# Kernel tuning notes

Measured on AMD Instinct MI355X. Metric: run time of the kernel, lower is better.

## Reference

```python
import jax, jax.numpy as jnp
import numpy as np

N_NODES = 50000
E_DIR = 250000
IN_FEATS = 256
N_HIDDEN = 64
N_CLASSES = 40
HEADS = 4
NEG_SLOPE = 0.2


def _build_graph():
    # mirrors to_undirected(edge_index) then add_self_loops(...)
    rng = np.random.default_rng(0)
    s = rng.integers(0, N_NODES, E_DIR)
    d = rng.integers(0, N_NODES, E_DIR)
    edges = np.stack([np.concatenate([s, d]), np.concatenate([d, s])], axis=0)
    edges = np.unique(edges, axis=1)  # dedup, as to_undirected does
    loops = np.arange(N_NODES)
    src = np.concatenate([edges[0], loops]).astype(np.int32)
    dst = np.concatenate([edges[1], loops]).astype(np.int32)
    return jnp.asarray(src), jnp.asarray(dst)


def setup_inputs() -> dict:
    key = jax.random.key(0)
    ks = jax.random.split(key, 16)
    src, dst = _build_graph()
    x = jax.random.uniform(ks[0], (N_NODES, IN_FEATS), dtype=jnp.float32)
    scale = 0.05
    # layer 0: IN -> HEADS*N_HIDDEN
    W0 = jax.random.normal(ks[1], (IN_FEATS, HEADS * N_HIDDEN), dtype=jnp.float32) * scale
    al0 = jax.random.normal(ks[2], (HEADS, N_HIDDEN), dtype=jnp.float32) * scale
    ar0 = jax.random.normal(ks[3], (HEADS, N_HIDDEN), dtype=jnp.float32) * scale
    b0 = jnp.zeros((HEADS * N_HIDDEN,), dtype=jnp.float32)
    # layer 1: HEADS*N_HIDDEN -> HEADS*N_HIDDEN
    W1 = jax.random.normal(ks[4], (HEADS * N_HIDDEN, HEADS * N_HIDDEN), dtype=jnp.float32) * scale
    al1 = jax.random.normal(ks[5], (HEADS, N_HIDDEN), dtype=jnp.float32) * scale
    ar1 = jax.random.normal(ks[6], (HEADS, N_HIDDEN), dtype=jnp.float32) * scale
    b1 = jnp.zeros((HEADS * N_HIDDEN,), dtype=jnp.float32)
    # layer 2: HEADS*N_HIDDEN -> HEADS*N_CLASSES (mean over heads at the end)
    W2 = jax.random.normal(ks[7], (HEADS * N_HIDDEN, HEADS * N_CLASSES), dtype=jnp.float32) * scale
    al2 = jax.random.normal(ks[8], (HEADS, N_CLASSES), dtype=jnp.float32) * scale
    ar2 = jax.random.normal(ks[9], (HEADS, N_CLASSES), dtype=jnp.float32) * scale
    b2 = jnp.zeros((HEADS * N_CLASSES,), dtype=jnp.float32)
    return {"x": x, "src": src, "dst": dst,
            "W0": W0, "al0": al0, "ar0": ar0, "b0": b0,
            "W1": W1, "al1": al1, "ar1": ar1, "b1": b1,
            "W2": W2, "al2": al2, "ar2": ar2, "b2": b2}


def _gat_layer(h, W, al, ar, b, src, dst):
    # DGL GATConv (no dropout, no residual): fc -> per-head attention -> edge softmax -> scatter-sum
    n = h.shape[0]
    nh, f = al.shape
    feat = (h @ W).reshape(n, nh, f)                      # [N,H,F]
    el = jnp.einsum('nhf,hf->nh', feat, al)               # [N,H]
    er = jnp.einsum('nhf,hf->nh', feat, ar)               # [N,H]
    e = jax.nn.leaky_relu(el[src] + er[dst], NEG_SLOPE)   # [E,H]
    emax = jax.lax.stop_gradient(jax.ops.segment_max(e, dst, num_segments=n))
    ee = jnp.exp(e - emax[dst])
    denom = jax.ops.segment_sum(ee, dst, num_segments=n)  # [N,H], >0 (self-loops)
    alpha = ee / denom[dst]                               # edge softmax over incoming edges
    msg = feat[src] * alpha[:, :, None]                   # [E,H,F]
    out = jax.ops.segment_sum(msg, dst, num_segments=n)   # [N,H,F]
    return out + b.reshape(1, nh, f)


def reference(x, src, dst, W0, al0, ar0, b0, W1, al1, ar1, b1, W2, al2, ar2, b2):
    n = x.shape[0]
    # x.shape[1] != 8189 -> row-normalize with clamp(min=1)
    h = x / jnp.clip(jnp.sum(x, axis=1, keepdims=True), 1.0)
    h = jax.nn.elu(_gat_layer(h, W0, al0, ar0, b0, src, dst)).reshape(n, -1)
    h = jax.nn.elu(_gat_layer(h, W1, al1, ar1, b1, src, dst)).reshape(n, -1)
    logits = _gat_layer(h, W2, al2, ar2, b2, src, dst).mean(axis=1)  # mean over heads
    return jax.nn.log_softmax(logits, axis=1)
```

## Files before the change

### kernel.cpp

```cpp
#include <hip/hip_runtime.h>
#include <math.h>

#define HEADS 4
#define HID 64
#define NCLS 40
#define IN_FEATS 256
#define NEG_SLOPE 0.2f
#define CAP 64
#define FP8_S 256.0f

typedef __attribute__((ext_vector_type(8))) short short8;
typedef __attribute__((ext_vector_type(4))) float floatx4;
typedef __attribute__((ext_vector_type(2))) float floatx2;

__device__ __forceinline__ ushort f2bf(float x) {
    union { float f; unsigned u; } v; v.f = x;
    unsigned r = (v.u + 0x7fff + ((v.u >> 16) & 1)) >> 16;
    return (ushort)r;
}
__device__ __forceinline__ unsigned char f2fp8(float x) {
    int pk = __builtin_amdgcn_cvt_pk_fp8_f32(x, x, 0, false);
    return (unsigned char)(pk & 0xff);
}
__device__ __forceinline__ void gload_lds16(const void* g, void* l) {
    __builtin_amdgcn_global_load_lds(
        (const __attribute__((address_space(1))) void*)g,
        (__attribute__((address_space(3))) void*)l, 16, 0, 0);
}

__global__ __launch_bounds__(256) void k_prep(const int* __restrict__ src,
                                              int* __restrict__ rowptr, int Em, int rb,
                                              const float* __restrict__ W0,
                                              const float* __restrict__ W1,
                                              const float* __restrict__ W2,
                                              ushort* __restrict__ Wt0,
                                              ushort* __restrict__ Wt1,
                                              ushort* __restrict__ Wt2,
                                              const float* __restrict__ al0,
                                              const float* __restrict__ ar0,
                                              const float* __restrict__ al1,
                                              const float* __restrict__ ar1,
                                              const float* __restrict__ al2,
                                              const float* __restrict__ ar2,
                                              ushort* __restrict__ Wel,
                                              const float* __restrict__ x,
                                              ushort* __restrict__ A16, int n) {
    int b = blockIdx.x;
    if (b < rb) {
        int j = b * 256 + threadIdx.x;
        if (j <= Em) {
            if (j == 0) {
                int hi = src[0];
                for (int v = 0; v <= hi; ++v) rowptr[v] = 0;
            } else if (j == Em) {
                int lo = src[Em - 1];
                for (int v = lo + 1; v <= n; ++v) rowptr[v] = Em;
            } else {
                int a = src[j - 1], c = src[j];
                for (int v = a + 1; v <= c; ++v) rowptr[v] = j;
            }
        }
        return;
    }
    b -= rb;
    if (b < 256) {
        int idx = b * 256 + threadIdx.x;
        int k = idx >> 8, c = idx & 255;
        Wt0[c * 256 + k] = f2bf(W0[idx]);
        Wt1[c * 256 + k] = f2bf(W1[idx]);
        if (idx < 40960) {
            int k2 = idx / 160, c2 = idx - k2 * 160;
            Wt2[c2 * 256 + k2] = f2bf(W2[idx]);
        }
        return;
    }
    b -= 256;
    if (b < 24) {
        int idx = b * 256 + threadIdx.x;
        int l = idx >> 11;
        int r = (idx >> 8) & 7;
        int k = idx & 255;
        int h = r & 3;
        bool isr = (r >= 4);
        const float* W  = (l == 0) ? W0 : (l == 1) ? W1 : W2;
        const float* av = isr ? ((l == 0) ? ar0 : (l == 1) ? ar1 : ar2)
                              : ((l == 0) ? al0 : (l == 1) ? al1 : al2);
        int F  = (l == 2) ? 40 : 64;
        int NC = (l == 2) ? 160 : 256;
        const float* wrow = W + (size_t)k * NC + h * F;
        const float* arow = av + h * F;
        float sum = 0.f;
        for (int f = 0; f < F; ++f) sum += wrow[f] * arow[f];
        Wel[idx] = f2bf(sum);
        return;
    }
    b -= 24;
    int row = b * 4 + (threadIdx.x >> 6);
    if (row >= n) return;
    int lane = threadIdx.x & 63;
    float4 v = reinterpret_cast<const float4*>(x + (size_t)row * 256)[lane];
    float s = v.x + v.y + v.z + v.w;
    for (int off = 32; off; off >>= 1) s += __shfl_down(s, off);
    s = __shfl(s, 0);
    float inv = 1.0f / fmaxf(s, 1.0f);
    ushort4 o;
    o.x = f2bf(v.x * inv); o.y = f2bf(v.y * inv);
    o.z = f2bf(v.z * inv); o.w = f2bf(v.w * inv);
    reinterpret_cast<ushort4*>(A16 + (size_t)row * 256)[lane] = o;
}

#define LDK 64
#define LDW 264

__global__ __launch_bounds__(256) void k_gemm_mfma(const ushort* __restrict__ A16,
                                                   const ushort* __restrict__ Wt,
                                                   const ushort* __restrict__ Welg,
                                                   unsigned char* __restrict__ Out8,
                                                   float* __restrict__ elv,
                                                   float* __restrict__ erv,
                                                   int n, int NCOL) {
    __shared__ ushort As[128 * LDK];
    __shared__ ushort Bs[128 * LDK];
    __shared__ ushort Wls[16 * LDW];
    int t = threadIdx.x;
    int lane = t & 63;
    int w = t >> 6;
    int wrow = (w & 1) * 64;
    int wcol = (w >> 1) * 64;
    int row0 = blockIdx.x * 128;
    int col0 = blockIdx.y * 128;
    int lrow = lane & 15;
    int kq = lane >> 4;
    bool fuse_blk = (blockIdx.y == 0);

    if (fuse_blk) {
        int r = t >> 5;
        int kk = (t & 31) * 8;
        uint4 v = *reinterpret_cast<const uint4*>(&Welg[r * 256 + kk]);
        *reinterpret_cast<uint4*>(&Wls[r * LDW + kk]) = v;
        *reinterpret_cast<uint4*>(&Wls[(r + 8) * LDW + kk]) = make_uint4(0u, 0u, 0u, 0u);
    }

    floatx4 acc[4][4];
    floatx4 acc_e[4];
#pragma unroll
    for (int i = 0; i < 4; ++i) {
        acc_e[i] = (floatx4)(0.f);
#pragma unroll
        for (int j = 0; j < 4; ++j) acc[i][j] = (floatx4)(0.f);
    }

    for (int k0 = 0; k0 < 256; k0 += 64) {
#pragma unroll
        for (int p = 0; p < 4; ++p) {
            int idx = p * 256 + t;
            int r = idx >> 3;
            int kk = (idx & 7) * 8;
            int gr = row0 + r; gr = (gr < n) ? gr : (n - 1);
            gload_lds16(&A16[(size_t)gr * 256 + k0 + kk], &As[idx * 8]);
        }
#pragma unroll
        for (int p = 0; p < 4; ++p) {
            int idx = p * 256 + t;
            int c = idx >> 3;
            int kk = (idx & 7) * 8;
            int gc = col0 + c; gc = (gc < NCOL) ? gc : (NCOL - 1);
            gload_lds16(&Wt[(size_t)gc * 256 + k0 + kk], &Bs[idx * 8]);
        }
        __syncthreads();

#pragma unroll
        for (int kc = 0; kc < 2; ++kc) {
            int kb = kc * 32 + kq * 8;
            short8 af[4], bf[4];
#pragma unroll
            for (int i = 0; i < 4; ++i)
                af[i] = *reinterpret_cast<const short8*>(&As[(wrow + 16 * i + lrow) * LDK + kb]);
#pragma unroll
            for (int j = 0; j < 4; ++j)
                bf[j] = *reinterpret_cast<const short8*>(&Bs[(wcol + 16 * j + lrow) * LDK + kb]);
#pragma unroll
            for (int i = 0; i < 4; ++i)
#pragma unroll
                for (int j = 0; j < 4; ++j)
                    acc[i][j] = __builtin_amdgcn_mfma_f32_16x16x32_bf16(af[i], bf[j], acc[i][j], 0, 0, 0);
            if (fuse_blk && wcol == 0) {
                short8 bw = *reinterpret_cast<const short8*>(&Wls[lrow * LDW + kb]);
#pragma unroll
                for (int i = 0; i < 4; ++i)
                    acc_e[i] = __builtin_amdgcn_mfma_f32_16x16x32_bf16(af[i], bw, acc_e[i], 0, 0, 0);
            }
        }
        __syncthreads();
    }

#pragma unroll
    for (int j = 0; j < 4; ++j) {
        int c = col0 + wcol + 16 * j + lrow;
        if (c >= NCOL) continue;
#pragma unroll
        for (int i = 0; i < 4; ++i) {
            int rbase = row0 + wrow + 16 * i + kq * 4;
#pragma unroll
            for (int r = 0; r < 4; ++r) {
                int gr = rbase + r;
                if (gr < n) Out8[(size_t)gr * NCOL + c] = f2fp8(acc[i][j][r] * FP8_S);
            }
        }
    }
    if (fuse_blk && wcol == 0 && lrow < 8) {
        bool is_er = (lrow >= 4);
        int h = lrow & 3;
#pragma unroll
        for (int i = 0; i < 4; ++i) {
            int rbase = row0 + wrow + 16 * i + kq * 4;
#pragma unroll
            for (int r = 0; r < 4; ++r) {
                int gr = rbase + r;
                if (gr < n) {
                    float v = acc_e[i][r];
                    if (is_er) erv[gr * 4 + h] = v;
                    else       elv[gr * 4 + h] = v;
                }
            }
        }
    }
}

template <int Fh, bool FINAL>
__global__ __launch_bounds__(256) void k_agg9(const unsigned char* __restrict__ F8,
                                              const float* __restrict__ el,
                                              const float* __restrict__ er,
                                              const int* __restrict__ rowptr,
                                              const int* __restrict__ dstv,
                                              const float* __restrict__ bias,
                                              ushort* __restrict__ out16,
                                              float* __restrict__ outF,
                                              int n) {
    constexpr int RL = 4 * Fh;
    constexpr bool FULL = (RL == 256);
    __shared__ float wls[4][CAP * 4];
    __shared__ int   mls[4][CAP];
    __shared__ float fbuf[4][FINAL ? 160 : 1];
    int wid = threadIdx.x >> 6;
    int node = blockIdx.x * 4 + wid;
    if (node >= n) node = n - 1;
    int lane = threadIdx.x & 63;
    int lo = rowptr[node];
    int deg_main = rowptr[node + 1] - lo;
    if (deg_main > CAP - 1) deg_main = CAP - 1;
    int deg = deg_main + 1;
    int degp = (deg + 7) & ~7;

    float* wl = wls[wid];
    int*   ml = mls[wid];

    int h = lane & 3;
    float ern = er[node * 4 + h];
    float wr[4];
    float s = 0.f;
    int ecount = 0;
    for (int e = lane >> 2; e < deg; e += 16) {
        int mid = (e < deg_main) ? dstv[lo + e] : node;
        if (h == 0) ml[e] = mid;
        float x = el[mid * 4 + h] + ern;
        x = (x > 0.f) ? x : NEG_SLOPE * x;
        float w = __expf(x);
        wr[ecount++] = w;
        s += w;
    }
#pragma unroll
    for (int off = 4; off < 64; off <<= 1) s += __shfl_xor(s, off);
    float invd = (1.0f / FP8_S) / s;
    {
        int e = lane >> 2;
        for (int i = 0; i < ecount; ++i, e += 16) wl[e * 4 + h] = wr[i] * invd;
    }
    if (lane < degp - deg) {
        int e = deg + lane;
        ml[e] = node;
        wl[e * 4 + 0] = 0.f; wl[e * 4 + 1] = 0.f;
        wl[e * 4 + 2] = 0.f; wl[e * 4 + 3] = 0.f;
    }
    asm volatile("s_waitcnt lgkmcnt(0)" ::: "memory");

    int my = 4 * lane;
    bool act = FULL || (my < RL);
    int hB = FULL ? (lane >> 4) : (my / Fh);
    const unsigned char* F8my = F8 + my;
    float a0 = 0.f, a1 = 0.f, a2 = 0.f, a3 = 0.f;
    for (int j0 = 0; j0 < degp; j0 += 8) {
        int4 mA = *reinterpret_cast<const int4*>(&ml[j0]);
        int4 mB = *reinterpret_cast<const int4*>(&ml[j0 + 4]);
        float w0 = wl[(j0 + 0) * 4 + hB], w1 = wl[(j0 + 1) * 4 + hB];
        float w2 = wl[(j0 + 2) * 4 + hB], w3 = wl[(j0 + 3) * 4 + hB];
        float w4 = wl[(j0 + 4) * 4 + hB], w5 = wl[(j0 + 5) * 4 + hB];
        float w6 = wl[(j0 + 6) * 4 + hB], w7 = wl[(j0 + 7) * 4 + hB];
        unsigned u0 = 0u, u1 = 0u, u2 = 0u, u3 = 0u;
        unsigned u4 = 0u, u5 = 0u, u6 = 0u, u7 = 0u;
        if (act) {
            u0 = *reinterpret_cast<const unsigned*>(&F8my[(size_t)mA.x * RL]);
            u1 = *reinterpret_cast<const unsigned*>(&F8my[(size_t)mA.y * RL]);
            u2 = *reinterpret_cast<const unsigned*>(&F8my[(size_t)mA.z * RL]);
            u3 = *reinterpret_cast<const unsigned*>(&F8my[(size_t)mA.w * RL]);
            u4 = *reinterpret_cast<const unsigned*>(&F8my[(size_t)mB.x * RL]);
            u5 = *reinterpret_cast<const unsigned*>(&F8my[(size_t)mB.y * RL]);
            u6 = *reinterpret_cast<const unsigned*>(&F8my[(size_t)mB.z * RL]);
            u7 = *reinterpret_cast<const unsigned*>(&F8my[(size_t)mB.w * RL]);
        }
#define ACC_EDGE(U, W)                                                     \
        {                                                                  \
            floatx2 p01 = __builtin_amdgcn_cvt_pk_f32_fp8(U, false);       \
            floatx2 p23 = __builtin_amdgcn_cvt_pk_f32_fp8(U, true);        \
            a0 = fmaf(W, p01.x, a0); a1 = fmaf(W, p01.y, a1);              \
            a2 = fmaf(W, p23.x, a2); a3 = fmaf(W, p23.y, a3);              \
        }
        ACC_EDGE(u0, w0) ACC_EDGE(u1, w1) ACC_EDGE(u2, w2) ACC_EDGE(u3, w3)
        ACC_EDGE(u4, w4) ACC_EDGE(u5, w5) ACC_EDGE(u6, w6) ACC_EDGE(u7, w7)
#undef ACC_EDGE
    }

    if (!FINAL) {
        if (act) {
            float4 b4 = *reinterpret_cast<const float4*>(&bias[my]);
            float o0 = a0 + b4.x, o1 = a1 + b4.y, o2 = a2 + b4.z, o3 = a3 + b4.w;
            o0 = (o0 > 0.f) ? o0 : (__expf(o0) - 1.0f);
            o1 = (o1 > 0.f) ? o1 : (__expf(o1) - 1.0f);
            o2 = (o2 > 0.f) ? o2 : (__expf(o2) - 1.0f);
            o3 = (o3 > 0.f) ? o3 : (__expf(o3) - 1.0f);
            uint2 pk;
            pk.x = (unsigned)f2bf(o0) | ((unsigned)f2bf(o1) << 16);
            pk.y = (unsigned)f2bf(o2) | ((unsigned)f2bf(o3) << 16);
            *reinterpret_cast<uint2*>(&out16[(size_t)node * RL + my]) = pk;
        }
    } else {
        if (act) {
            float4 b4 = *reinterpret_cast<const float4*>(&bias[my]);
            fbuf[wid][my + 0] = a0 + b4.x;
            fbuf[wid][my + 1] = a1 + b4.y;
            fbuf[wid][my + 2] = a2 + b4.z;
            fbuf[wid][my + 3] = a3 + b4.w;
        }
        asm volatile("s_waitcnt lgkmcnt(0)" ::: "memory");
        float val = 0.f;
        if (lane < 40)
            val = 0.25f * (fbuf[wid][lane] + fbuf[wid][40 + lane] +
                           fbuf[wid][80 + lane] + fbuf[wid][120 + lane]);
        float mx = (lane < 40) ? val : -1e30f;
#pragma unroll
        for (int off = 32; off; off >>= 1) mx = fmaxf(mx, __shfl_xor(mx, off));
        float ex = (lane < 40) ? __expf(val - mx) : 0.f;
        float se = ex;
#pragma unroll
        for (int off = 32; off; off >>= 1) se += __shfl_xor(se, off);
        if (lane < 40) outF[(size_t)node * 40 + lane] = val - mx - logf(se);
    }
}

extern "C" void kernel_launch(void* const* d_in, const int* in_sizes, int n_in,
                              void* d_out, int out_size, void* d_ws, size_t ws_size,
                              hipStream_t stream) {
    const float* x  = (const float*)d_in[0];
    const int* src  = (const int*)d_in[1];
    const int* dst  = (const int*)d_in[2];
    const float* W0 = (const float*)d_in[3];
    const float* al0 = (const float*)d_in[4];
    const float* ar0 = (const float*)d_in[5];
    const float* b0 = (const float*)d_in[6];
    const float* W1 = (const float*)d_in[7];
    const float* al1 = (const float*)d_in[8];
    const float* ar1 = (const float*)d_in[9];
    const float* b1 = (const float*)d_in[10];
    const float* W2 = (const float*)d_in[11];
    const float* al2 = (const float*)d_in[12];
    const float* ar2 = (const float*)d_in[13];
    const float* b2 = (const float*)d_in[14];
    float* out = (float*)d_out;

    const int n = in_sizes[0] / IN_FEATS;
    const int E = in_sizes[1];
    const int Em = E - n;

    char* base = (char*)d_ws;
    size_t off = 0;
    auto alloc = [&](size_t bytes) {
        void* p = base + off;
        off = (off + bytes + 255) & ~(size_t)255;
        return p;
    };
    ushort* A16 = (ushort*)alloc((size_t)n * 256 * 2);
    unsigned char* F8 = (unsigned char*)alloc((size_t)n * 256);
    ushort* Wt0 = (ushort*)alloc((size_t)256 * 256 * 2);
    ushort* Wt1 = (ushort*)alloc((size_t)256 * 256 * 2);
    ushort* Wt2 = (ushort*)alloc((size_t)160 * 256 * 2);
    ushort* Wel = (ushort*)alloc((size_t)3 * 8 * 256 * 2);
    float* el  = (float*)alloc((size_t)n * HEADS * 4);
    float* er  = (float*)alloc((size_t)n * HEADS * 4);
    int* rowptr = (int*)alloc((size_t)(n + 1) * 4);
    (void)ws_size; (void)n_in; (void)out_size;

    const int rb = (Em + 1 + 255) / 256;
    const int nb4 = (n + 3) / 4;
    const int gemm_rows = (n + 127) / 128;

    k_prep<<<rb + 256 + 24 + nb4, 256, 0, stream>>>(src, rowptr, Em, rb,
                                                    W0, W1, W2, Wt0, Wt1, Wt2,
                                                    al0, ar0, al1, ar1, al2, ar2,
                                                    Wel, x, A16, n);

    k_gemm_mfma<<<dim3(gemm_rows, 2), 256, 0, stream>>>(A16, Wt0, Wel, F8, el, er, n, 256);
    k_agg9<HID, false><<<nb4, 256, 0, stream>>>(F8, el, er, rowptr, dst, b0, A16, out, n);

    k_gemm_mfma<<<dim3(gemm_rows, 2), 256, 0, stream>>>(A16, Wt1, Wel + 2048, F8, el, er, n, 256);
    k_agg9<HID, false><<<nb4, 256, 0, stream>>>(F8, el, er, rowptr, dst, b1, A16, out, n);

    k_gemm_mfma<<<dim3(gemm_rows, 2), 256, 0, stream>>>(A16, Wt2, Wel + 4096, F8, el, er, n, 160);
    k_agg9<NCLS, true><<<nb4, 256, 0, stream>>>(F8, el, er, rowptr, dst, b2, nullptr, out, n);
}
```

Measured before the change: 273.8 us.

## Split edges across half-waves with 8-byte FP8 gathers and software-pipelined loads

For the full-width (256-feature) aggregation layers, each lane now gathers 8 FP8 features per neighbor, and the two half-waves process alternating groups of 4 edges. Partial sums are combined with a cross-half shuffle. Loads for the next batch of edges are double-buffered so they overlap with the FMAs of the current batch. This aims to increase gather width and memory-level parallelism, at the cost of more registers, an extra shuffle reduction, and only half the lanes doing the epilogue.

```diff
diff --git a/kernel.cpp b/kernel.cpp
--- a/kernel.cpp
+++ b/kernel.cpp
@@ -284,56 +284,124 @@
     }
     asm volatile("s_waitcnt lgkmcnt(0)" ::: "memory");
 
-    int my = 4 * lane;
-    bool act = FULL || (my < RL);
-    int hB = FULL ? (lane >> 4) : (my / Fh);
-    const unsigned char* F8my = F8 + my;
-    float a0 = 0.f, a1 = 0.f, a2 = 0.f, a3 = 0.f;
-    for (int j0 = 0; j0 < degp; j0 += 8) {
-        int4 mA = *reinterpret_cast<const int4*>(&ml[j0]);
-        int4 mB = *reinterpret_cast<const int4*>(&ml[j0 + 4]);
-        float w0 = wl[(j0 + 0) * 4 + hB], w1 = wl[(j0 + 1) * 4 + hB];
-        float w2 = wl[(j0 + 2) * 4 + hB], w3 = wl[(j0 + 3) * 4 + hB];
-        float w4 = wl[(j0 + 4) * 4 + hB], w5 = wl[(j0 + 5) * 4 + hB];
-        float w6 = wl[(j0 + 6) * 4 + hB], w7 = wl[(j0 + 7) * 4 + hB];
-        unsigned u0 = 0u, u1 = 0u, u2 = 0u, u3 = 0u;
-        unsigned u4 = 0u, u5 = 0u, u6 = 0u, u7 = 0u;
-        if (act) {
-            u0 = *reinterpret_cast<const unsigned*>(&F8my[(size_t)mA.x * RL]);
-            u1 = *reinterpret_cast<const unsigned*>(&F8my[(size_t)mA.y * RL]);
-            u2 = *reinterpret_cast<const unsigned*>(&F8my[(size_t)mA.z * RL]);
-            u3 = *reinterpret_cast<const unsigned*>(&F8my[(size_t)mA.w * RL]);
-            u4 = *reinterpret_cast<const unsigned*>(&F8my[(size_t)mB.x * RL]);
-            u5 = *reinterpret_cast<const unsigned*>(&F8my[(size_t)mB.y * RL]);
-            u6 = *reinterpret_cast<const unsigned*>(&F8my[(size_t)mB.z * RL]);
-            u7 = *reinterpret_cast<const unsigned*>(&F8my[(size_t)mB.w * RL]);
-        }
-#define ACC_EDGE(U, W)                                                     \
-        {                                                                  \
-            floatx2 p01 = __builtin_amdgcn_cvt_pk_f32_fp8(U, false);       \
-            floatx2 p23 = __builtin_amdgcn_cvt_pk_f32_fp8(U, true);        \
-            a0 = fmaf(W, p01.x, a0); a1 = fmaf(W, p01.y, a1);              \
-            a2 = fmaf(W, p23.x, a2); a3 = fmaf(W, p23.y, a3);              \
-        }
-        ACC_EDGE(u0, w0) ACC_EDGE(u1, w1) ACC_EDGE(u2, w2) ACC_EDGE(u3, w3)
-        ACC_EDGE(u4, w4) ACC_EDGE(u5, w5) ACC_EDGE(u6, w6) ACC_EDGE(u7, w7)
-#undef ACC_EDGE
-    }
-
-    if (!FINAL) {
-        if (act) {
-            float4 b4 = *reinterpret_cast<const float4*>(&bias[my]);
-            float o0 = a0 + b4.x, o1 = a1 + b4.y, o2 = a2 + b4.z, o3 = a3 + b4.w;
+    if constexpr (FULL) {
+        int ep4 = (lane >> 5) << 2;
+        int c8 = (lane & 31) * 8;
+        int hB2 = c8 >> 6;
+        const unsigned char* F8c = F8 + c8;
+        float a0 = 0.f, a1 = 0.f, a2 = 0.f, a3 = 0.f;
+        float a4 = 0.f, a5 = 0.f, a6 = 0.f, a7 = 0.f;
+        int nb = degp >> 3;
+
+#define LOADB(J, MI, W0, W1, W2, W3, U0, U1, U2, U3)                        \
+        {                                                                   \
+            MI = *reinterpret_cast<const int4*>(&ml[(J) + ep4]);            \
+            W0 = wl[((J) + ep4 + 0) * 4 + hB2];                             \
+            W1 = wl[((J) + ep4 + 1) * 4 + hB2];                             \
+            W2 = wl[((J) + ep4 + 2) * 4 + hB2];                             \
+            W3 = wl[((J) + ep4 + 3) * 4 + hB2];                             \
+            U0 = *reinterpret_cast<const uint2*>(&F8c[(size_t)MI.x * 256]); \
+            U1 = *reinterpret_cast<const uint2*>(&F8c[(size_t)MI.y * 256]); \
+            U2 = *reinterpret_cast<const uint2*>(&F8c[(size_t)MI.z * 256]); \
+            U3 = *reinterpret_cast<const uint2*>(&F8c[(size_t)MI.w * 256]); \
+        }
+#define FMA8(W, U)                                                          \
+        {                                                                   \
+            floatx2 p01 = __builtin_amdgcn_cvt_pk_f32_fp8((U).x, false);    \
+            floatx2 p23 = __builtin_amdgcn_cvt_pk_f32_fp8((U).x, true);     \
+            floatx2 p45 = __builtin_amdgcn_cvt_pk_f32_fp8((U).y, false);    \
+            floatx2 p67 = __builtin_amdgcn_cvt_pk_f32_fp8((U).y, true);     \
+            a0 = fmaf(W, p01.x, a0); a1 = fmaf(W, p01.y, a1);               \
+            a2 = fmaf(W, p23.x, a2); a3 = fmaf(W, p23.y, a3);               \
+            a4 = fmaf(W, p45.x, a4); a5 = fmaf(W, p45.y, a5);               \
+            a6 = fmaf(W, p67.x, a6); a7 = fmaf(W, p67.y, a7);               \
+        }
+#define FMABATCH(W0, W1, W2, W3, U0, U1, U2, U3)                            \
+        { FMA8(W0, U0) FMA8(W1, U1) FMA8(W2, U2) FMA8(W3, U3) }
+
+        int4 miA, miB;
+        float wA0, wA1, wA2, wA3, wB0, wB1, wB2, wB3;
+        uint2 uA0, uA1, uA2, uA3, uB0, uB1, uB2, uB3;
+
+        LOADB(0, miA, wA0, wA1, wA2, wA3, uA0, uA1, uA2, uA3)
+        for (int b = 1; b < nb; ++b) {
+            int j0 = b * 8;
+            if (b & 1) {
+                LOADB(j0, miB, wB0, wB1, wB2, wB3, uB0, uB1, uB2, uB3)
+                FMABATCH(wA0, wA1, wA2, wA3, uA0, uA1, uA2, uA3)
+            } else {
+                LOADB(j0, miA, wA0, wA1, wA2, wA3, uA0, uA1, uA2, uA3)
+                FMABATCH(wB0, wB1, wB2, wB3, uB0, uB1, uB2, uB3)
+            }
+        }
+        if (nb & 1) { FMABATCH(wA0, wA1, wA2, wA3, uA0, uA1, uA2, uA3) }
+        else        { FMABATCH(wB0, wB1, wB2, wB3, uB0, uB1, uB2, uB3) }
+#undef FMABATCH
+#undef FMA8
+#undef LOADB
+
+        a0 += __shfl_xor(a0, 32); a1 += __shfl_xor(a1, 32);
+        a2 += __shfl_xor(a2, 32); a3 += __shfl_xor(a3, 32);
+        a4 += __shfl_xor(a4, 32); a5 += __shfl_xor(a5, 32);
+        a6 += __shfl_xor(a6, 32); a7 += __shfl_xor(a7, 32);
+
+        if (lane < 32) {
+            float4 b4a = *reinterpret_cast<const float4*>(&bias[c8]);
+            float4 b4b = *reinterpret_cast<const float4*>(&bias[c8 + 4]);
+            float o0 = a0 + b4a.x, o1 = a1 + b4a.y, o2 = a2 + b4a.z, o3 = a3 + b4a.w;
+            float o4 = a4 + b4b.x, o5 = a5 + b4b.y, o6 = a6 + b4b.z, o7 = a7 + b4b.w;
             o0 = (o0 > 0.f) ? o0 : (__expf(o0) - 1.0f);
             o1 = (o1 > 0.f) ? o1 : (__expf(o1) - 1.0f);
             o2 = (o2 > 0.f) ? o2 : (__expf(o2) - 1.0f);
             o3 = (o3 > 0.f) ? o3 : (__expf(o3) - 1.0f);
-            uint2 pk;
+            o4 = (o4 > 0.f) ? o4 : (__expf(o4) - 1.0f);
+            o5 = (o5 > 0.f) ? o5 : (__expf(o5) - 1.0f);
+            o6 = (o6 > 0.f) ? o6 : (__expf(o6) - 1.0f);
+            o7 = (o7 > 0.f) ? o7 : (__expf(o7) - 1.0f);
+            uint4 pk;
             pk.x = (unsigned)f2bf(o0) | ((unsigned)f2bf(o1) << 16);
             pk.y = (unsigned)f2bf(o2) | ((unsigned)f2bf(o3) << 16);
-            *reinterpret_cast<uint2*>(&out16[(size_t)node * RL + my]) = pk;
+            pk.z = (unsigned)f2bf(o4) | ((unsigned)f2bf(o5) << 16);
+            pk.w = (unsigned)f2bf(o6) | ((unsigned)f2bf(o7) << 16);
+            *reinterpret_cast<uint4*>(&out16[(size_t)node * RL + c8]) = pk;
         }
     } else {
+        int my = 4 * lane;
+        bool act = (my < RL);
+        int hB = my / Fh;
+        const unsigned char* F8my = F8 + my;
+        float a0 = 0.f, a1 = 0.f, a2 = 0.f, a3 = 0.f;
+        for (int j0 = 0; j0 < degp; j0 += 8) {
+            int4 mA = *reinterpret_cast<const int4*>(&ml[j0]);
+            int4 mB = *reinterpret_cast<const int4*>(&ml[j0 + 4]);
+            float w0 = wl[(j0 + 0) * 4 + hB], w1 = wl[(j0 + 1) * 4 + hB];
+            float w2 = wl[(j0 + 2) * 4 + hB], w3 = wl[(j0 + 3) * 4 + hB];
+            float w4 = wl[(j0 + 4) * 4 + hB], w5 = wl[(j0 + 5) * 4 + hB];
+            float w6 = wl[(j0 + 6) * 4 + hB], w7 = wl[(j0 + 7) * 4 + hB];
+            unsigned u0 = 0u, u1 = 0u, u2 = 0u, u3 = 0u;
+            unsigned u4 = 0u, u5 = 0u, u6 = 0u, u7 = 0u;
+            if (act) {
+                u0 = *reinterpret_cast<const unsigned*>(&F8my[(size_t)mA.x * RL]);
+                u1 = *reinterpret_cast<const unsigned*>(&F8my[(size_t)mA.y * RL]);
+                u2 = *reinterpret_cast<const unsigned*>(&F8my[(size_t)mA.z * RL]);
+                u3 = *reinterpret_cast<const unsigned*>(&F8my[(size_t)mA.w * RL]);
+                u4 = *reinterpret_cast<const unsigned*>(&F8my[(size_t)mB.x * RL]);
+                u5 = *reinterpret_cast<const unsigned*>(&F8my[(size_t)mB.y * RL]);
+                u6 = *reinterpret_cast<const unsigned*>(&F8my[(size_t)mB.z * RL]);
+                u7 = *reinterpret_cast<const unsigned*>(&F8my[(size_t)mB.w * RL]);
+            }
+#define ACC_EDGE(U, W)                                                     \
+            {                                                              \
+                floatx2 p01 = __builtin_amdgcn_cvt_pk_f32_fp8(U, false);   \
+                floatx2 p23 = __builtin_amdgcn_cvt_pk_f32_fp8(U, true);    \
+                a0 = fmaf(W, p01.x, a0); a1 = fmaf(W, p01.y, a1);          \
+                a2 = fmaf(W, p23.x, a2); a3 = fmaf(W, p23.y, a3);          \
+            }
+            ACC_EDGE(u0, w0) ACC_EDGE(u1, w1) ACC_EDGE(u2, w2) ACC_EDGE(u3, w3)
+            ACC_EDGE(u4, w4) ACC_EDGE(u5, w5) ACC_EDGE(u6, w6) ACC_EDGE(u7, w7)
+#undef ACC_EDGE
+        }
+
         if (act) {
             float4 b4 = *reinterpret_cast<const float4*>(&bias[my]);
             fbuf[wid][my + 0] = a0 + b4.x;
```

After: 295.6 us. 8.0% more time.
